# Kernel tuning notes

Measured on AMD Instinct MI355X. Metric: run time of the kernel, lower is better.

Reference implementation:

```python
import jax, jax.numpy as jnp
import numpy as np

B, T, N, D, H, NMASK = 8192, 2, 40, 64, 1, 3
EPS = 1e-5


def setup_inputs() -> dict:
    key = jax.random.key(0)
    ks = jax.random.split(key, 12)
    F = T * N * 2 * D  # flattened feature size fed to BatchNorm1d
    return {
        "x": jax.random.normal(ks[0], (B, N, D), jnp.float32),
        "masker": jax.random.uniform(ks[1], (T, NMASK, N, N), jnp.float32, -0.27, 0.27),  # xavier-like
        "ln_gamma": jnp.ones((N,), jnp.float32),
        "ln_beta": jnp.zeros((N,), jnp.float32),
        "gnn_w": jax.random.normal(ks[2], (1, T, H, 2 * D, D), jnp.float32) * 0.05,
        "gnn_b": jax.random.normal(ks[3], (T, H, N, D), jnp.float32) * 0.05,
        "bn_gamma": jnp.ones((H, F), jnp.float32),
        "bn_beta": jnp.zeros((H, F), jnp.float32),
        "bn_mean": jax.random.normal(ks[4], (H, F), jnp.float32) * 0.1,
        "bn_var": jax.random.uniform(ks[5], (H, F), jnp.float32, 0.5, 1.5),
        "gate_w": jax.random.normal(ks[6], (N * D, N), jnp.float32) * 0.02,
        "gate_b": jnp.zeros((N,), jnp.float32),
    }


def reference(x, masker, ln_gamma, ln_beta, gnn_w, gnn_b, bn_gamma, bn_beta, bn_mean, bn_var, gate_w, gate_b):
    b = x.shape[0]
    # broadcast input to towers: (B, T, N, D)
    h = jnp.broadcast_to(x[:, None], (b, T, N, D))
    # adjacency from product of mask matrices: (T, N, N)
    adj = jax.nn.relu(jnp.prod(masker, axis=1))
    mask = (adj != 0).astype(x.dtype)
    # LayerNorm(num_fields) applied on transposed adj == normalize over rows (axis -2)
    mu = adj.mean(axis=-2, keepdims=True)
    var = adj.var(axis=-2, keepdims=True)
    ln = (adj - mu) / jnp.sqrt(var + EPS) * ln_gamma[:, None] + ln_beta[:, None]
    x_masked = ln + (1.0 - mask) * (-1e9) + jnp.eye(N, dtype=x.dtype)
    # softmax over rows (dim=1 of (T,N,N)) then re-mask
    A = jax.nn.softmax(x_masked, axis=1) * mask  # (T, N, N)
    for idx in range(H):
        # nei[b,t,n,d] = sum_m h[b,t,m,d] * A[t,m,n]
        nei = jnp.einsum('btmd,tmn->btnd', h, A)
        hc = jnp.concatenate([h, nei], axis=-1)  # (B,T,N,2D)
        flat = hc.reshape(b, -1)
        flat = (flat - bn_mean[idx]) / jnp.sqrt(bn_var[idx] + EPS) * bn_gamma[idx] + bn_beta[idx]
        hc = flat.reshape(b, T, N, 2 * D)
        # per-tower transform: (B,T,N,2D) x (T,2D,D) -> (B,T,N,D)
        h = jnp.einsum('btnf,tfd->btnd', hc, gnn_w[0, :, idx]) + gnn_b[:, idx]
    # attention pooling over fields
    logits = h.reshape(b, T, N * D) @ gate_w + gate_b  # (B,T,N)
    w = jax.nn.softmax(logits, axis=2)
    return jnp.sum(h * w[..., None], axis=2)  # (B, T, D)
```

## Files before the change

kernel.cpp:

```cpp
#include <hip/hip_runtime.h>
#include <hip/hip_bf16.h>
#include <stdint.h>

typedef float v4f __attribute__((ext_vector_type(4)));
typedef short v8s __attribute__((ext_vector_type(8)));

#define NB 40

__device__ __forceinline__ unsigned short f2b(float f) {
  __hip_bfloat16 h = __float2bfloat16(f);
  unsigned short u;
  __builtin_memcpy(&u, &h, 2);
  return u;
}
__device__ __forceinline__ unsigned pk2(float lo, float hi) {
  __hip_bfloat162 h = __float22bfloat162_rn(make_float2(lo, hi));
  unsigned u;
  __builtin_memcpy(&u, &h, 4);
  return u;
}
__device__ __forceinline__ float b2f16(unsigned short h) {
  return __uint_as_float(((unsigned)h) << 16);
}
__device__ __forceinline__ float blo(unsigned u) { return __uint_as_float(u << 16); }
__device__ __forceinline__ float bhi(unsigned u) { return __uint_as_float(u & 0xFFFF0000u); }


__global__ __launch_bounds__(256) void prep(
    const float* __restrict__ masker,
    const float* __restrict__ ln_gamma, const float* __restrict__ ln_beta,
    const float* __restrict__ gnn_w, const float* __restrict__ gnn_b,
    const float* __restrict__ bn_gamma, const float* __restrict__ bn_beta,
    const float* __restrict__ bn_mean, const float* __restrict__ bn_var,
    const float* __restrict__ gate_w,
    unsigned short* __restrict__ A1pk, unsigned short* __restrict__ W2pk,
    unsigned short* __restrict__ Gpk, float* __restrict__ s1,
    float* __restrict__ sNT, float* __restrict__ bias2T)
{
  const int tid = threadIdx.x;
  if (blockIdx.x == 0) {
    __shared__ float AtL[2 * NB * NB];
    const int w = tid >> 6, lane = tid & 63;
    #pragma unroll 1
    for (int it = 0; it < 20; ++it) {
      const int c = it * 4 + w;
      const int t = c / NB, n = c % NB;
      const int m = lane;
      float adj = 0.f;
      if (m < NB) {
        float p = masker[((t*3+0)*NB+m)*NB+n]
                * masker[((t*3+1)*NB+m)*NB+n]
                * masker[((t*3+2)*NB+m)*NB+n];
        adj = p > 0.f ? p : 0.f;
      }
      float s = adj;
      #pragma unroll
      for (int d = 1; d < 64; d <<= 1) s += __shfl_xor(s, d);
      const float mu = s * (1.f/NB);
      const float dv = (m < NB) ? adj - mu : 0.f;
      float v2 = dv * dv;
      #pragma unroll
      for (int d = 1; d < 64; d <<= 1) v2 += __shfl_xor(v2, d);
      const float inv = rsqrtf(v2 * (1.f/NB) + 1e-5f);
      float val = -3.0e38f;
      if (m < NB) {
        float lnv = dv * inv * ln_gamma[m] + ln_beta[m];
        val = lnv + (adj != 0.f ? 0.f : -1e9f) + (m == n ? 1.f : 0.f);
      }
      float mx = val;
      #pragma unroll
      for (int d = 1; d < 64; d <<= 1) mx = fmaxf(mx, __shfl_xor(mx, d));
      const float e = (m < NB) ? __expf(val - mx) : 0.f;
      float es = e;
      #pragma unroll
      for (int d = 1; d < 64; d <<= 1) es += __shfl_xor(es, d);
      if (m < NB)
        AtL[(t*NB+n)*NB + m] = (adj != 0.f) ? e / es : 0.f;
    }
    __syncthreads();
    for (int e = tid; e < 6144; e += 256) {
      int frag = e >> 9, rem = e & 511, lane2 = rem >> 3, jj = rem & 7;
      int t = frag / 6, r2 = frag % 6, nt = r2 >> 1, ks = r2 & 1;
      int n = nt*16 + (lane2 & 15);
      int m = ks*32 + (lane2 >> 4)*8 + jj;
      A1pk[e] = f2b((n < NB && m < NB) ? AtL[(t*NB+n)*NB+m] : 0.f);
    }
  } else {
    const int gid = (blockIdx.x - 1) * 256 + tid, gsz = 63 * 256;
    for (int e = gid; e < 16384; e += gsz) {
      int frag = e >> 9, rem = e & 511, lane = rem >> 3, jj = rem & 7;
      int t = frag >> 4, ks = (frag >> 2) & 3, dt = frag & 3;
      int f = ks*32 + (lane >> 4)*8 + jj, d = dt*16 + (lane & 15);
      W2pk[e] = f2b(gnn_w[t*8192 + f*64 + d]);
    }
    for (int e = gid; e < 122880; e += gsz) {
      int frag = e >> 9, rem = e & 511, lane = rem >> 3, jj = rem & 7;
      int kt = frag / 3, jt = frag % 3;
      int fl = kt*32 + (lane >> 4)*8 + jj, j = jt*16 + (lane & 15);
      Gpk[e] = f2b(j < NB ? gate_w[fl*NB + j] : 0.f);
    }
    for (int e = gid; e < 5120; e += gsz) {
      int t = e / 2560, n = (e % 2560) / 64, d = e & 63;
      int F = (t*NB + n)*128 + d;
      s1[e] = bn_gamma[F] * rsqrtf(bn_var[F] + 1e-5f);
    }
    for (int e = gid; e < 5120; e += gsz) {
      int t = e / 2560, d = (e % 2560) / 40, n = e % 40;
      int F = (t*NB + n)*128 + 64 + d;
      sNT[e] = bn_gamma[F] * rsqrtf(bn_var[F] + 1e-5f);
    }
    for (int e4 = gid; e4 < 20480; e4 += gsz) {
      int e = e4 >> 2, part = e4 & 3;
      int t = e / 2560, d = (e % 2560) / 40, n = e % 40;
      float acc = (part == 0) ? gnn_b[(t*NB + n)*64 + d] : 0.f;
      int Fb = (t*NB + n)*128;
      int f0 = part * 32;
      for (int f = f0; f < f0 + 32; ++f) {
        float s = bn_gamma[Fb+f] * rsqrtf(bn_var[Fb+f] + 1e-5f);
        float o = bn_beta[Fb+f] - bn_mean[Fb+f] * s;
        acc += o * gnn_w[t*8192 + f*64 + d];
      }
      acc += __shfl_xor(acc, 1);
      acc += __shfl_xor(acc, 2);
      if (part == 0) bias2T[e] = acc;
    }
  }
}

__global__ __launch_bounds__(256) void kernelM(
    const float* __restrict__ x,
    const unsigned short* __restrict__ A1pk, const unsigned short* __restrict__ W2pk,
    const unsigned short* __restrict__ Gpk, const float* __restrict__ s1,
    const float* __restrict__ sNT, const float* __restrict__ bias2T,
    const float* __restrict__ gate_b, float* __restrict__ out)
{
  __shared__ __align__(16) unsigned short hc[160 * 136];
  __shared__ float pj[16 * 48];

  const int tid = threadIdx.x;
  const int lane = tid & 63;
  const int w = tid >> 6;
  const int l = lane & 15, q = lane >> 4;
  const int b0 = blockIdx.x * 4;
  unsigned* hcU = (unsigned*)hc;
  unsigned short* hL = hc;

  uint4 xr[5];
  #pragma unroll
  for (int it = 0; it < 5; ++it) {
    const int c = it * 256 + tid, row = c >> 3, dp8 = c & 7;
    const float* xp = x + (size_t)b0 * 2560 + row * 64 + dp8 * 8;
    const float4 f0 = *(const float4*)xp;
    const float4 f1 = *(const float4*)(xp + 4);
    xr[it] = make_uint4(pk2(f0.x, f0.y), pk2(f0.z, f0.w),
                        pk2(f1.x, f1.y), pk2(f1.z, f1.w));
  }
  if (tid < 12) hcU[5120 + tid] = 0u;
  #pragma unroll
  for (int it = 0; it < 5; ++it) {
    const int c = it * 256 + tid, row = c >> 3, dp8 = c & 7;
    const int bq = row / NB, n = row - bq * NB;
    unsigned short* base = hc + (bq * 64 + dp8 * 8) * NB + n;
    const unsigned uu0 = xr[it].x, uu1 = xr[it].y, uu2 = xr[it].z, uu3 = xr[it].w;
    base[0*NB] = (unsigned short)(uu0 & 0xFFFF);
    base[1*NB] = (unsigned short)(uu0 >> 16);
    base[2*NB] = (unsigned short)(uu1 & 0xFFFF);
    base[3*NB] = (unsigned short)(uu1 >> 16);
    base[4*NB] = (unsigned short)(uu2 & 0xFFFF);
    base[5*NB] = (unsigned short)(uu2 >> 16);
    base[6*NB] = (unsigned short)(uu3 & 0xFFFF);
    base[7*NB] = (unsigned short)(uu3 >> 16);
  }
  __syncthreads();
  v8s b1[4][2];
  #pragma unroll
  for (int i = 0; i < 4; ++i)
    #pragma unroll
    for (int ks = 0; ks < 2; ++ks)
      b1[i][ks] = *(const v8s*)(hc + ((w * 4 + i) * 16 + l) * NB + ks * 32 + q * 8);
  __syncthreads();

  #pragma unroll
  for (int t = 0; t < 2; ++t) {
    if (t) __syncthreads();

    v8s a1[3][2], w2[4];
    #pragma unroll
    for (int nt = 0; nt < 3; ++nt)
      #pragma unroll
      for (int ks = 0; ks < 2; ++ks)
        a1[nt][ks] = *(const v8s*)(A1pk + (((t*3 + nt)*2 + ks) << 9) + lane*8);
    #pragma unroll
    for (int ks = 0; ks < 4; ++ks)
      w2[ks] = *(const v8s*)(W2pk + (((t*4 + ks)*4 + w) << 9) + lane*8);

    #pragma unroll
    for (int it = 0; it < 5; ++it) {
      const int c = it*256 + tid;
      const int row = c >> 3, dp8 = c & 7;
      const uint4 xv = xr[it];
      const int n = row % NB;
      const float4 sA = *(const float4*)(s1 + (t*NB + n)*64 + dp8*8);
      const float4 sB = *(const float4*)(s1 + (t*NB + n)*64 + dp8*8 + 4);
      uint4 p;
      p.x = pk2(blo(xv.x)*sA.x, bhi(xv.x)*sA.y);
      p.y = pk2(blo(xv.y)*sA.z, bhi(xv.y)*sA.w);
      p.z = pk2(blo(xv.z)*sB.x, bhi(xv.z)*sB.y);
      p.w = pk2(blo(xv.w)*sB.z, bhi(xv.w)*sB.w);
      *(uint4*)(hcU + row*68 + dp8*4) = p;
    }
    #pragma unroll
    for (int i = 0; i < 4; ++i) {
      const int R = (w*4+i)*16 + l;
      const int bb = R >> 6, d = R & 63;
      #pragma unroll
      for (int nt = 0; nt < 3; ++nt) {
        v4f acc = {0.f, 0.f, 0.f, 0.f};
        acc = __builtin_amdgcn_mfma_f32_16x16x32_bf16(a1[nt][0], b1[i][0], acc, 0, 0, 0);
        acc = __builtin_amdgcn_mfma_f32_16x16x32_bf16(a1[nt][1], b1[i][1], acc, 0, 0, 0);
        const float4 sv = *(const float4*)(sNT + (t*64+d)*40 + nt*16 + q*4);
        #pragma unroll
        for (int r = 0; r < 4; ++r) {
          int n = nt*16 + q*4 + r;
          if (n < NB) hc[(bb*NB + n)*136 + 64 + d] = f2b(acc[r]*sv[r]);
        }
      }
    }
    __syncthreads();
    unsigned pkr0[10], pkr1[10];
    #pragma unroll
    for (int mt = 0; mt < 10; ++mt) {
      v4f acc = {0.f, 0.f, 0.f, 0.f};
      #pragma unroll
      for (int ks = 0; ks < 4; ++ks) {
        v8s af = *(const v8s*)(hc + (mt*16 + l)*136 + ks*32 + q*8);
        acc = __builtin_amdgcn_mfma_f32_16x16x32_bf16(af, w2[ks], acc, 0, 0, 0);
      }
      const int d = w*16 + l;
      const int G = mt*16 + q*4;
      const int bb = G / NB, n0 = G - bb*NB;
      const float4 bv = *(const float4*)(bias2T + (t*64+d)*40 + n0);
      pkr0[mt] = pk2(acc[0] + bv.x, acc[1] + bv.y);
      pkr1[mt] = pk2(acc[2] + bv.z, acc[3] + bv.w);
    }
    __syncthreads();
    #pragma unroll
    for (int mt = 0; mt < 10; ++mt) {
      const int d = w*16 + l;
      const int G = mt*16 + q*4;
      const int bb = G / NB, n0 = G - bb*NB;
      hL[bb*2568 + (n0+0)*64 + d] = (unsigned short)(pkr0[mt] & 0xFFFF);
      hL[bb*2568 + (n0+1)*64 + d] = (unsigned short)(pkr0[mt] >> 16);
      hL[bb*2568 + (n0+2)*64 + d] = (unsigned short)(pkr1[mt] & 0xFFFF);
      hL[bb*2568 + (n0+3)*64 + d] = (unsigned short)(pkr1[mt] >> 16);
    }
    __syncthreads();
    v4f ac0 = {0,0,0,0}, ac1 = {0,0,0,0}, ac2 = {0,0,0,0};
    for (int kt = w; kt < 80; kt += 4) {
      v8s bf = *(const v8s*)(hL + (l & 3)*2568 + kt*32 + q*8);
      v8s g0 = *(const v8s*)(Gpk + ((kt*3+0) << 9) + lane*8);
      v8s g1 = *(const v8s*)(Gpk + ((kt*3+1) << 9) + lane*8);
      v8s g2 = *(const v8s*)(Gpk + ((kt*3+2) << 9) + lane*8);
      ac0 = __builtin_amdgcn_mfma_f32_16x16x32_bf16(g0, bf, ac0, 0, 0, 0);
      ac1 = __builtin_amdgcn_mfma_f32_16x16x32_bf16(g1, bf, ac1, 0, 0, 0);
      ac2 = __builtin_amdgcn_mfma_f32_16x16x32_bf16(g2, bf, ac2, 0, 0, 0);
    }
    if (l < 4) {
      #pragma unroll
      for (int r = 0; r < 4; ++r) {
        pj[(w*4 + l)*48 +  0 + q*4 + r] = ac0[r];
        pj[(w*4 + l)*48 + 16 + q*4 + r] = ac1[r];
        pj[(w*4 + l)*48 + 32 + q*4 + r] = ac2[r];
      }
    }
    __syncthreads();
    {
      float v = -3.0e38f;
      if (lane < NB) {
        v = gate_b[lane];
        #pragma unroll
        for (int ww = 0; ww < 4; ++ww) v += pj[(ww*4 + w)*48 + lane];
      }
      float mx = v;
      #pragma unroll
      for (int m = 1; m < 64; m <<= 1) mx = fmaxf(mx, __shfl_xor(mx, m));
      float e = (lane < NB) ? __expf(v - mx) : 0.f;
      float es = e;
      #pragma unroll
      for (int m = 1; m < 64; m <<= 1) es += __shfl_xor(es, m);
      const float wgt = e / es;
      float accp = 0.f;
      #pragma unroll
      for (int n = 0; n < NB; ++n)
        accp += b2f16(hL[w*2568 + n*64 + lane]) * __shfl(wgt, n);
      out[((size_t)(b0 + w)*2 + t)*64 + lane] = accp;
    }
  }
}

extern "C" void kernel_launch(void* const* d_in, const int* in_sizes, int n_in,
                              void* d_out, int out_size, void* d_ws, size_t ws_size,
                              hipStream_t stream) {
  const float* x        = (const float*)d_in[0];
  const float* masker   = (const float*)d_in[1];
  const float* ln_gamma = (const float*)d_in[2];
  const float* ln_beta  = (const float*)d_in[3];
  const float* gnn_w    = (const float*)d_in[4];
  const float* gnn_b    = (const float*)d_in[5];
  const float* bn_gamma = (const float*)d_in[6];
  const float* bn_beta  = (const float*)d_in[7];
  const float* bn_mean  = (const float*)d_in[8];
  const float* bn_var   = (const float*)d_in[9];
  const float* gate_w   = (const float*)d_in[10];
  const float* gate_b   = (const float*)d_in[11];
  float* out = (float*)d_out;

  char* ws = (char*)d_ws;
  unsigned short* A1pk   = (unsigned short*)(ws + 0);
  unsigned short* W2pk   = (unsigned short*)(ws + 12288);
  unsigned short* Gpk    = (unsigned short*)(ws + 45056);
  float*          s1     = (float*)(ws + 290816);
  float*          sNT    = (float*)(ws + 311296);
  float*          bias2T = (float*)(ws + 331904);

  prep<<<64, 256, 0, stream>>>(masker, ln_gamma, ln_beta, gnn_w, gnn_b,
                               bn_gamma, bn_beta, bn_mean, bn_var, gate_w,
                               A1pk, W2pk, Gpk, s1, sNT, bias2T);
  kernelM<<<2048, 256, 0, stream>>>(x, A1pk, W2pk, Gpk,
                                    s1, sNT, bias2T, gate_b, out);
}
```

Baseline: 239.8 us.

## Split fused kernel into transform and gate-pooling kernels via global intermediate

The single fused kernel is split in two. The first computes the per-tower transformed features and writes them as bf16 to a global workspace buffer. The second handles 16 batch rows per block, so each Gpk gate-weight fragment loaded feeds 16 useful MFMA columns instead of 4, and it software-pipelines the global loads ahead of the MFMAs. The cost is an extra global write and read of the intermediate (about 84 MB of bf16) plus one more kernel launch.

```diff
diff --git a/kernel.cpp b/kernel.cpp
--- a/kernel.cpp
+++ b/kernel.cpp
@@ -127,15 +127,13 @@
   }
 }
 
-__global__ __launch_bounds__(256) void kernelM(
+__global__ __launch_bounds__(256) void kernelA(
     const float* __restrict__ x,
     const unsigned short* __restrict__ A1pk, const unsigned short* __restrict__ W2pk,
-    const unsigned short* __restrict__ Gpk, const float* __restrict__ s1,
-    const float* __restrict__ sNT, const float* __restrict__ bias2T,
-    const float* __restrict__ gate_b, float* __restrict__ out)
+    const float* __restrict__ s1, const float* __restrict__ sNT,
+    const float* __restrict__ bias2T, unsigned short* __restrict__ hLg)
 {
   __shared__ __align__(16) unsigned short hc[160 * 136];
-  __shared__ float pj[16 * 48];
 
   const int tid = threadIdx.x;
   const int lane = tid & 63;
@@ -143,7 +141,6 @@
   const int l = lane & 15, q = lane >> 4;
   const int b0 = blockIdx.x * 4;
   unsigned* hcU = (unsigned*)hc;
-  unsigned short* hL = hc;
 
   uint4 xr[5];
   #pragma unroll
@@ -227,7 +224,6 @@
       }
     }
     __syncthreads();
-    unsigned pkr0[10], pkr1[10];
     #pragma unroll
     for (int mt = 0; mt < 10; ++mt) {
       v4f acc = {0.f, 0.f, 0.f, 0.f};
@@ -240,60 +236,99 @@
       const int G = mt*16 + q*4;
       const int bb = G / NB, n0 = G - bb*NB;
       const float4 bv = *(const float4*)(bias2T + (t*64+d)*40 + n0);
-      pkr0[mt] = pk2(acc[0] + bv.x, acc[1] + bv.y);
-      pkr1[mt] = pk2(acc[2] + bv.z, acc[3] + bv.w);
-    }
+      unsigned short* hp = hLg + ((size_t)(b0 + bb)*2 + t)*2560 + n0*64 + d;
+      hp[0*64] = f2b(acc[0] + bv.x);
+      hp[1*64] = f2b(acc[1] + bv.y);
+      hp[2*64] = f2b(acc[2] + bv.z);
+      hp[3*64] = f2b(acc[3] + bv.w);
+    }
+  }
+}
+
+__global__ __launch_bounds__(512) void kernelB(
+    const unsigned short* __restrict__ hLg, const unsigned short* __restrict__ Gpk,
+    const float* __restrict__ gate_b, float* __restrict__ out)
+{
+  __shared__ float pj[8 * 48 * 17];
+  __shared__ float wgt[16 * NB];
+
+  const int tid = threadIdx.x;
+  const int w = tid >> 6, lane = tid & 63;
+  const int l = lane & 15, q = lane >> 4;
+  const int b0 = blockIdx.x * 16;
+
+  v4f ac[2][3];
+  #pragma unroll
+  for (int t = 0; t < 2; ++t)
+    #pragma unroll
+    for (int jt = 0; jt < 3; ++jt)
+      ac[t][jt] = (v4f){0.f, 0.f, 0.f, 0.f};
+
+  const unsigned short* hb = hLg + (size_t)(b0 + l) * 2 * 2560 + q * 8;
+  int kt = w;
+  v8s g0 = *(const v8s*)(Gpk + ((kt*3+0) << 9) + lane*8);
+  v8s g1 = *(const v8s*)(Gpk + ((kt*3+1) << 9) + lane*8);
+  v8s g2 = *(const v8s*)(Gpk + ((kt*3+2) << 9) + lane*8);
+  v8s bf0 = *(const v8s*)(hb + kt*32);
+  v8s bf1 = *(const v8s*)(hb + 2560 + kt*32);
+  #pragma unroll
+  for (int i = 0; i < 10; ++i) {
+    const int ktn = kt + 8;
+    v8s ng0, ng1, ng2, nbf0, nbf1;
+    if (i < 9) {
+      ng0  = *(const v8s*)(Gpk + ((ktn*3+0) << 9) + lane*8);
+      ng1  = *(const v8s*)(Gpk + ((ktn*3+1) << 9) + lane*8);
+      ng2  = *(const v8s*)(Gpk + ((ktn*3+2) << 9) + lane*8);
+      nbf0 = *(const v8s*)(hb + ktn*32);
+      nbf1 = *(const v8s*)(hb + 2560 + ktn*32);
+    }
+    ac[0][0] = __builtin_amdgcn_mfma_f32_16x16x32_bf16(g0, bf0, ac[0][0], 0, 0, 0);
+    ac[0][1] = __builtin_amdgcn_mfma_f32_16x16x32_bf16(g1, bf0, ac[0][1], 0, 0, 0);
+    ac[0][2] = __builtin_amdgcn_mfma_f32_16x16x32_bf16(g2, bf0, ac[0][2], 0, 0, 0);
+    ac[1][0] = __builtin_amdgcn_mfma_f32_16x16x32_bf16(g0, bf1, ac[1][0], 0, 0, 0);
+    ac[1][1] = __builtin_amdgcn_mfma_f32_16x16x32_bf16(g1, bf1, ac[1][1], 0, 0, 0);
+    ac[1][2] = __builtin_amdgcn_mfma_f32_16x16x32_bf16(g2, bf1, ac[1][2], 0, 0, 0);
+    g0 = ng0; g1 = ng1; g2 = ng2; bf0 = nbf0; bf1 = nbf1;
+    kt = ktn;
+  }
+
+  #pragma unroll
+  for (int t = 0; t < 2; ++t) {
+    if (t) __syncthreads();
+    #pragma unroll
+    for (int jt = 0; jt < 3; ++jt)
+      #pragma unroll
+      for (int r = 0; r < 4; ++r)
+        pj[(w*48 + jt*16 + q*4 + r)*17 + l] = ac[t][jt][r];
     __syncthreads();
     #pragma unroll
-    for (int mt = 0; mt < 10; ++mt) {
-      const int d = w*16 + l;
-      const int G = mt*16 + q*4;
-      const int bb = G / NB, n0 = G - bb*NB;
-      hL[bb*2568 + (n0+0)*64 + d] = (unsigned short)(pkr0[mt] & 0xFFFF);
-      hL[bb*2568 + (n0+1)*64 + d] = (unsigned short)(pkr0[mt] >> 16);
-      hL[bb*2568 + (n0+2)*64 + d] = (unsigned short)(pkr1[mt] & 0xFFFF);
-      hL[bb*2568 + (n0+3)*64 + d] = (unsigned short)(pkr1[mt] >> 16);
-    }
-    __syncthreads();
-    v4f ac0 = {0,0,0,0}, ac1 = {0,0,0,0}, ac2 = {0,0,0,0};
-    for (int kt = w; kt < 80; kt += 4) {
-      v8s bf = *(const v8s*)(hL + (l & 3)*2568 + kt*32 + q*8);
-      v8s g0 = *(const v8s*)(Gpk + ((kt*3+0) << 9) + lane*8);
-      v8s g1 = *(const v8s*)(Gpk + ((kt*3+1) << 9) + lane*8);
-      v8s g2 = *(const v8s*)(Gpk + ((kt*3+2) << 9) + lane*8);
-      ac0 = __builtin_amdgcn_mfma_f32_16x16x32_bf16(g0, bf, ac0, 0, 0, 0);
-      ac1 = __builtin_amdgcn_mfma_f32_16x16x32_bf16(g1, bf, ac1, 0, 0, 0);
-      ac2 = __builtin_amdgcn_mfma_f32_16x16x32_bf16(g2, bf, ac2, 0, 0, 0);
-    }
-    if (l < 4) {
-      #pragma unroll
-      for (int r = 0; r < 4; ++r) {
-        pj[(w*4 + l)*48 +  0 + q*4 + r] = ac0[r];
-        pj[(w*4 + l)*48 + 16 + q*4 + r] = ac1[r];
-        pj[(w*4 + l)*48 + 32 + q*4 + r] = ac2[r];
-      }
-    }
-    __syncthreads();
-    {
+    for (int hb2 = 0; hb2 < 2; ++hb2) {
+      const int b = w*2 + hb2;
       float v = -3.0e38f;
       if (lane < NB) {
         v = gate_b[lane];
         #pragma unroll
-        for (int ww = 0; ww < 4; ++ww) v += pj[(ww*4 + w)*48 + lane];
+        for (int w8 = 0; w8 < 8; ++w8) v += pj[(w8*48 + lane)*17 + b];
       }
       float mx = v;
       #pragma unroll
       for (int m = 1; m < 64; m <<= 1) mx = fmaxf(mx, __shfl_xor(mx, m));
-      float e = (lane < NB) ? __expf(v - mx) : 0.f;
+      const float e = (lane < NB) ? __expf(v - mx) : 0.f;
       float es = e;
       #pragma unroll
       for (int m = 1; m < 64; m <<= 1) es += __shfl_xor(es, m);
-      const float wgt = e / es;
-      float accp = 0.f;
-      #pragma unroll
+      if (lane < NB) wgt[b*NB + lane] = e / es;
+    }
+    __syncthreads();
+    #pragma unroll
+    for (int hb2 = 0; hb2 < 2; ++hb2) {
+      const int b = w*2 + hb2;
+      const unsigned short* hp = hLg + ((size_t)(b0 + b)*2 + t)*2560 + lane;
+      float a = 0.f;
+      #pragma unroll 8
       for (int n = 0; n < NB; ++n)
-        accp += b2f16(hL[w*2568 + n*64 + lane]) * __shfl(wgt, n);
-      out[((size_t)(b0 + w)*2 + t)*64 + lane] = accp;
+        a += b2f16(hp[n*64]) * wgt[b*NB + n];
+      out[((size_t)(b0 + b)*2 + t)*64 + lane] = a;
     }
   }
 }
@@ -322,10 +357,11 @@
   float*          s1     = (float*)(ws + 290816);
   float*          sNT    = (float*)(ws + 311296);
   float*          bias2T = (float*)(ws + 331904);
+  unsigned short* hLg    = (unsigned short*)(ws + 352384);
 
   prep<<<64, 256, 0, stream>>>(masker, ln_gamma, ln_beta, gnn_w, gnn_b,
                                bn_gamma, bn_beta, bn_mean, bn_var, gate_w,
                                A1pk, W2pk, Gpk, s1, sNT, bias2T);
-  kernelM<<<2048, 256, 0, stream>>>(x, A1pk, W2pk, Gpk,
-                                    s1, sNT, bias2T, gate_b, out);
-}
+  kernelA<<<2048, 256, 0, stream>>>(x, A1pk, W2pk, s1, sNT, bias2T, hLg);
+  kernelB<<<512, 512, 0, stream>>>(hLg, Gpk, gate_b, out);
+}
```

Result: slower. 244.9 us (+2.1%).

## Split towers across blocks and software-pipeline gate GEMM loads

Applied to the files above, without the earlier changes.

Each block now handles a single tower (t taken from the low bit of blockIdx) rather than looping over both towers, so the grid doubles to 4096 blocks. The gate-logit loop is fully unrolled and double-buffers its Gpk and hL fragment loads two iterations ahead of the MFMAs, and the final pooling loop is unrolled by 8. The aim is more parallelism and hidden load latency. The cost is that every block reloads x, converts it to bf16 and runs the first transpose for only half the work, which doubles x global reads.

```diff
diff --git a/kernel.cpp b/kernel.cpp
--- a/kernel.cpp
+++ b/kernel.cpp
@@ -141,7 +141,8 @@
   const int lane = tid & 63;
   const int w = tid >> 6;
   const int l = lane & 15, q = lane >> 4;
-  const int b0 = blockIdx.x * 4;
+  const int t = blockIdx.x & 1;
+  const int b0 = (blockIdx.x >> 1) * 4;
   unsigned* hcU = (unsigned*)hc;
   unsigned short* hL = hc;
 
@@ -180,121 +181,133 @@
       b1[i][ks] = *(const v8s*)(hc + ((w * 4 + i) * 16 + l) * NB + ks * 32 + q * 8);
   __syncthreads();
 
-  #pragma unroll
-  for (int t = 0; t < 2; ++t) {
-    if (t) __syncthreads();
-
-    v8s a1[3][2], w2[4];
-    #pragma unroll
-    for (int nt = 0; nt < 3; ++nt)
-      #pragma unroll
-      for (int ks = 0; ks < 2; ++ks)
-        a1[nt][ks] = *(const v8s*)(A1pk + (((t*3 + nt)*2 + ks) << 9) + lane*8);
-    #pragma unroll
-    for (int ks = 0; ks < 4; ++ks)
-      w2[ks] = *(const v8s*)(W2pk + (((t*4 + ks)*4 + w) << 9) + lane*8);
-
-    #pragma unroll
-    for (int it = 0; it < 5; ++it) {
-      const int c = it*256 + tid;
-      const int row = c >> 3, dp8 = c & 7;
-      const uint4 xv = xr[it];
-      const int n = row % NB;
-      const float4 sA = *(const float4*)(s1 + (t*NB + n)*64 + dp8*8);
-      const float4 sB = *(const float4*)(s1 + (t*NB + n)*64 + dp8*8 + 4);
-      uint4 p;
-      p.x = pk2(blo(xv.x)*sA.x, bhi(xv.x)*sA.y);
-      p.y = pk2(blo(xv.y)*sA.z, bhi(xv.y)*sA.w);
-      p.z = pk2(blo(xv.z)*sB.x, bhi(xv.z)*sB.y);
-      p.w = pk2(blo(xv.w)*sB.z, bhi(xv.w)*sB.w);
-      *(uint4*)(hcU + row*68 + dp8*4) = p;
-    }
-    #pragma unroll
-    for (int i = 0; i < 4; ++i) {
-      const int R = (w*4+i)*16 + l;
-      const int bb = R >> 6, d = R & 63;
-      #pragma unroll
-      for (int nt = 0; nt < 3; ++nt) {
-        v4f acc = {0.f, 0.f, 0.f, 0.f};
-        acc = __builtin_amdgcn_mfma_f32_16x16x32_bf16(a1[nt][0], b1[i][0], acc, 0, 0, 0);
-        acc = __builtin_amdgcn_mfma_f32_16x16x32_bf16(a1[nt][1], b1[i][1], acc, 0, 0, 0);
-        const float4 sv = *(const float4*)(sNT + (t*64+d)*40 + nt*16 + q*4);
-        #pragma unroll
-        for (int r = 0; r < 4; ++r) {
-          int n = nt*16 + q*4 + r;
-          if (n < NB) hc[(bb*NB + n)*136 + 64 + d] = f2b(acc[r]*sv[r]);
-        }
-      }
-    }
-    __syncthreads();
-    unsigned pkr0[10], pkr1[10];
-    #pragma unroll
-    for (int mt = 0; mt < 10; ++mt) {
+  v8s a1[3][2], w2[4];
+  #pragma unroll
+  for (int nt = 0; nt < 3; ++nt)
+    #pragma unroll
+    for (int ks = 0; ks < 2; ++ks)
+      a1[nt][ks] = *(const v8s*)(A1pk + (((t*3 + nt)*2 + ks) << 9) + lane*8);
+  #pragma unroll
+  for (int ks = 0; ks < 4; ++ks)
+    w2[ks] = *(const v8s*)(W2pk + (((t*4 + ks)*4 + w) << 9) + lane*8);
+
+  #pragma unroll
+  for (int it = 0; it < 5; ++it) {
+    const int c = it*256 + tid;
+    const int row = c >> 3, dp8 = c & 7;
+    const uint4 xv = xr[it];
+    const int n = row % NB;
+    const float4 sA = *(const float4*)(s1 + (t*NB + n)*64 + dp8*8);
+    const float4 sB = *(const float4*)(s1 + (t*NB + n)*64 + dp8*8 + 4);
+    uint4 p;
+    p.x = pk2(blo(xv.x)*sA.x, bhi(xv.x)*sA.y);
+    p.y = pk2(blo(xv.y)*sA.z, bhi(xv.y)*sA.w);
+    p.z = pk2(blo(xv.z)*sB.x, bhi(xv.z)*sB.y);
+    p.w = pk2(blo(xv.w)*sB.z, bhi(xv.w)*sB.w);
+    *(uint4*)(hcU + row*68 + dp8*4) = p;
+  }
+  #pragma unroll
+  for (int i = 0; i < 4; ++i) {
+    const int R = (w*4+i)*16 + l;
+    const int bb = R >> 6, d = R & 63;
+    #pragma unroll
+    for (int nt = 0; nt < 3; ++nt) {
       v4f acc = {0.f, 0.f, 0.f, 0.f};
-      #pragma unroll
-      for (int ks = 0; ks < 4; ++ks) {
-        v8s af = *(const v8s*)(hc + (mt*16 + l)*136 + ks*32 + q*8);
-        acc = __builtin_amdgcn_mfma_f32_16x16x32_bf16(af, w2[ks], acc, 0, 0, 0);
-      }
-      const int d = w*16 + l;
-      const int G = mt*16 + q*4;
-      const int bb = G / NB, n0 = G - bb*NB;
-      const float4 bv = *(const float4*)(bias2T + (t*64+d)*40 + n0);
-      pkr0[mt] = pk2(acc[0] + bv.x, acc[1] + bv.y);
-      pkr1[mt] = pk2(acc[2] + bv.z, acc[3] + bv.w);
-    }
-    __syncthreads();
-    #pragma unroll
-    for (int mt = 0; mt < 10; ++mt) {
-      const int d = w*16 + l;
-      const int G = mt*16 + q*4;
-      const int bb = G / NB, n0 = G - bb*NB;
-      hL[bb*2568 + (n0+0)*64 + d] = (unsigned short)(pkr0[mt] & 0xFFFF);
-      hL[bb*2568 + (n0+1)*64 + d] = (unsigned short)(pkr0[mt] >> 16);
-      hL[bb*2568 + (n0+2)*64 + d] = (unsigned short)(pkr1[mt] & 0xFFFF);
-      hL[bb*2568 + (n0+3)*64 + d] = (unsigned short)(pkr1[mt] >> 16);
-    }
-    __syncthreads();
-    v4f ac0 = {0,0,0,0}, ac1 = {0,0,0,0}, ac2 = {0,0,0,0};
-    for (int kt = w; kt < 80; kt += 4) {
-      v8s bf = *(const v8s*)(hL + (l & 3)*2568 + kt*32 + q*8);
-      v8s g0 = *(const v8s*)(Gpk + ((kt*3+0) << 9) + lane*8);
-      v8s g1 = *(const v8s*)(Gpk + ((kt*3+1) << 9) + lane*8);
-      v8s g2 = *(const v8s*)(Gpk + ((kt*3+2) << 9) + lane*8);
-      ac0 = __builtin_amdgcn_mfma_f32_16x16x32_bf16(g0, bf, ac0, 0, 0, 0);
-      ac1 = __builtin_amdgcn_mfma_f32_16x16x32_bf16(g1, bf, ac1, 0, 0, 0);
-      ac2 = __builtin_amdgcn_mfma_f32_16x16x32_bf16(g2, bf, ac2, 0, 0, 0);
-    }
-    if (l < 4) {
+      acc = __builtin_amdgcn_mfma_f32_16x16x32_bf16(a1[nt][0], b1[i][0], acc, 0, 0, 0);
+      acc = __builtin_amdgcn_mfma_f32_16x16x32_bf16(a1[nt][1], b1[i][1], acc, 0, 0, 0);
+      const float4 sv = *(const float4*)(sNT + (t*64+d)*40 + nt*16 + q*4);
       #pragma unroll
       for (int r = 0; r < 4; ++r) {
-        pj[(w*4 + l)*48 +  0 + q*4 + r] = ac0[r];
-        pj[(w*4 + l)*48 + 16 + q*4 + r] = ac1[r];
-        pj[(w*4 + l)*48 + 32 + q*4 + r] = ac2[r];
-      }
-    }
-    __syncthreads();
-    {
-      float v = -3.0e38f;
-      if (lane < NB) {
-        v = gate_b[lane];
-        #pragma unroll
-        for (int ww = 0; ww < 4; ++ww) v += pj[(ww*4 + w)*48 + lane];
-      }
-      float mx = v;
-      #pragma unroll
-      for (int m = 1; m < 64; m <<= 1) mx = fmaxf(mx, __shfl_xor(mx, m));
-      float e = (lane < NB) ? __expf(v - mx) : 0.f;
-      float es = e;
-      #pragma unroll
-      for (int m = 1; m < 64; m <<= 1) es += __shfl_xor(es, m);
-      const float wgt = e / es;
-      float accp = 0.f;
-      #pragma unroll
-      for (int n = 0; n < NB; ++n)
-        accp += b2f16(hL[w*2568 + n*64 + lane]) * __shfl(wgt, n);
-      out[((size_t)(b0 + w)*2 + t)*64 + lane] = accp;
-    }
+        int n = nt*16 + q*4 + r;
+        if (n < NB) hc[(bb*NB + n)*136 + 64 + d] = f2b(acc[r]*sv[r]);
+      }
+    }
+  }
+  __syncthreads();
+  unsigned pkr0[10], pkr1[10];
+  #pragma unroll
+  for (int mt = 0; mt < 10; ++mt) {
+    v4f acc = {0.f, 0.f, 0.f, 0.f};
+    #pragma unroll
+    for (int ks = 0; ks < 4; ++ks) {
+      v8s af = *(const v8s*)(hc + (mt*16 + l)*136 + ks*32 + q*8);
+      acc = __builtin_amdgcn_mfma_f32_16x16x32_bf16(af, w2[ks], acc, 0, 0, 0);
+    }
+    const int d = w*16 + l;
+    const int G = mt*16 + q*4;
+    const int bb = G / NB, n0 = G - bb*NB;
+    const float4 bv = *(const float4*)(bias2T + (t*64+d)*40 + n0);
+    pkr0[mt] = pk2(acc[0] + bv.x, acc[1] + bv.y);
+    pkr1[mt] = pk2(acc[2] + bv.z, acc[3] + bv.w);
+  }
+  __syncthreads();
+  #pragma unroll
+  for (int mt = 0; mt < 10; ++mt) {
+    const int d = w*16 + l;
+    const int G = mt*16 + q*4;
+    const int bb = G / NB, n0 = G - bb*NB;
+    hL[bb*2568 + (n0+0)*64 + d] = (unsigned short)(pkr0[mt] & 0xFFFF);
+    hL[bb*2568 + (n0+1)*64 + d] = (unsigned short)(pkr0[mt] >> 16);
+    hL[bb*2568 + (n0+2)*64 + d] = (unsigned short)(pkr1[mt] & 0xFFFF);
+    hL[bb*2568 + (n0+3)*64 + d] = (unsigned short)(pkr1[mt] >> 16);
+  }
+  __syncthreads();
+  v4f ac0 = {0,0,0,0}, ac1 = {0,0,0,0}, ac2 = {0,0,0,0};
+  {
+    v8s pg0[2], pg1[2], pg2[2], pbf[2];
+    #pragma unroll
+    for (int s = 0; s < 2; ++s) {
+      const int kt = w + s*4;
+      pg0[s] = *(const v8s*)(Gpk + ((kt*3+0) << 9) + lane*8);
+      pg1[s] = *(const v8s*)(Gpk + ((kt*3+1) << 9) + lane*8);
+      pg2[s] = *(const v8s*)(Gpk + ((kt*3+2) << 9) + lane*8);
+      pbf[s] = *(const v8s*)(hL + (l & 3)*2568 + kt*32 + q*8);
+    }
+    #pragma unroll
+    for (int i = 0; i < 20; ++i) {
+      const int cur = i & 1;
+      const v8s G0 = pg0[cur], G1 = pg1[cur], G2 = pg2[cur], BF = pbf[cur];
+      if (i < 18) {
+        const int ktn = w + (i+2)*4;
+        pg0[cur] = *(const v8s*)(Gpk + ((ktn*3+0) << 9) + lane*8);
+        pg1[cur] = *(const v8s*)(Gpk + ((ktn*3+1) << 9) + lane*8);
+        pg2[cur] = *(const v8s*)(Gpk + ((ktn*3+2) << 9) + lane*8);
+        pbf[cur] = *(const v8s*)(hL + (l & 3)*2568 + ktn*32 + q*8);
+      }
+      ac0 = __builtin_amdgcn_mfma_f32_16x16x32_bf16(G0, BF, ac0, 0, 0, 0);
+      ac1 = __builtin_amdgcn_mfma_f32_16x16x32_bf16(G1, BF, ac1, 0, 0, 0);
+      ac2 = __builtin_amdgcn_mfma_f32_16x16x32_bf16(G2, BF, ac2, 0, 0, 0);
+    }
+  }
+  if (l < 4) {
+    #pragma unroll
+    for (int r = 0; r < 4; ++r) {
+      pj[(w*4 + l)*48 +  0 + q*4 + r] = ac0[r];
+      pj[(w*4 + l)*48 + 16 + q*4 + r] = ac1[r];
+      pj[(w*4 + l)*48 + 32 + q*4 + r] = ac2[r];
+    }
+  }
+  __syncthreads();
+  {
+    float v = -3.0e38f;
+    if (lane < NB) {
+      v = gate_b[lane];
+      #pragma unroll
+      for (int ww = 0; ww < 4; ++ww) v += pj[(ww*4 + w)*48 + lane];
+    }
+    float mx = v;
+    #pragma unroll
+    for (int m = 1; m < 64; m <<= 1) mx = fmaxf(mx, __shfl_xor(mx, m));
+    float e = (lane < NB) ? __expf(v - mx) : 0.f;
+    float es = e;
+    #pragma unroll
+    for (int m = 1; m < 64; m <<= 1) es += __shfl_xor(es, m);
+    const float wgt = e / es;
+    float accp = 0.f;
+    #pragma unroll 8
+    for (int n = 0; n < NB; ++n)
+      accp += b2f16(hL[w*2568 + n*64 + lane]) * __shfl(wgt, n);
+    out[((size_t)(b0 + w)*2 + t)*64 + lane] = accp;
   }
 }
 
@@ -326,6 +339,6 @@
   prep<<<64, 256, 0, stream>>>(masker, ln_gamma, ln_beta, gnn_w, gnn_b,
                                bn_gamma, bn_beta, bn_mean, bn_var, gate_w,
                                A1pk, W2pk, Gpk, s1, sNT, bias2T);
-  kernelM<<<2048, 256, 0, stream>>>(x, A1pk, W2pk, Gpk,
+  kernelM<<<4096, 256, 0, stream>>>(x, A1pk, W2pk, Gpk,
                                     s1, sNT, bias2T, gate_b, out);
 }
```

Result: no change. 238.4 us (-0.6%).
